# Performance work log

Measured on AMD Instinct MI355X. Metric: run time of the kernel, lower is better.

## Reference

```python
import jax, jax.numpy as jnp
import numpy as np
from jax import lax

VOCAB = 32000
D_MODEL = 1024
N_LAYERS = 4
D_STATE = 8
D_CONV = 4
EXPAND = 2
D_INNER = EXPAND * D_MODEL          # 2048
DT_RANK = (D_MODEL + 15) // 16      # 64
B, L = 2, 1024


def setup_inputs() -> dict:
    key = jax.random.key(0)
    ks = jax.random.split(key, 20)
    s = 0.02
    inp = {
        "input_ids": jax.random.randint(ks[0], (B, L), 0, VOCAB, dtype=jnp.int32),
        "embed": jax.random.normal(ks[1], (VOCAB, D_MODEL), jnp.float32) * s,
        "in_proj_w": jax.random.normal(ks[2], (N_LAYERS, 2 * D_INNER, D_MODEL), jnp.float32) * s,
        "conv_w": jax.random.normal(ks[3], (N_LAYERS, D_INNER, 1, D_CONV), jnp.float32) * s,
        "conv_b": jnp.zeros((N_LAYERS, D_INNER), jnp.float32),
        "x_proj_w": jax.random.normal(ks[4], (N_LAYERS, DT_RANK + 2 * D_STATE, D_INNER), jnp.float32) * s,
        "dt_proj_w": jax.random.normal(ks[5], (N_LAYERS, D_INNER, DT_RANK), jnp.float32) * s,
        "dt_proj_b": jax.random.normal(ks[6], (N_LAYERS, D_INNER), jnp.float32) * 0.1,
        "A_log": jnp.broadcast_to(jnp.log(jnp.arange(1, D_STATE + 1, dtype=jnp.float32)),
                                  (N_LAYERS, D_INNER, D_STATE)) + 0.0,
        "D": jnp.ones((N_LAYERS, D_INNER), jnp.float32),
        "out_proj_w": jax.random.normal(ks[7], (N_LAYERS, D_MODEL, D_INNER), jnp.float32) * s,
        "ln_g": jnp.ones((N_LAYERS, D_MODEL), jnp.float32),
        "ln_b": jnp.zeros((N_LAYERS, D_MODEL), jnp.float32),
        "fn_g": jnp.ones((D_MODEL,), jnp.float32),
        "fn_b": jnp.zeros((D_MODEL,), jnp.float32),
        "fc_w": jax.random.normal(ks[8], (VOCAB, D_MODEL), jnp.float32) * s,
        "fc_b": jnp.zeros((VOCAB,), jnp.float32),
    }
    return inp


def layer_norm(x, g, b, eps=1e-5):
    mu = jnp.mean(x, -1, keepdims=True)
    var = jnp.var(x, -1, keepdims=True)
    return (x - mu) * lax.rsqrt(var + eps) * g + b


def silu(x):
    return x * jax.nn.sigmoid(x)


def selective_scan(deltaA, deltaBu, C):
    # deltaA, deltaBu: (b,l,d,n); C: (b,l,n) -> y: (b,l,d)
    def step(h, inp):
        dA, dBu, c = inp
        h = dA * h + dBu                       # (b,d,n)
        y = jnp.einsum('bdn,bn->bd', h, c)
        return h, y
    h0 = jnp.zeros(deltaA.shape[:1] + deltaA.shape[2:], deltaA.dtype)
    _, ys = lax.scan(step, h0, (deltaA.transpose(1, 0, 2, 3),
                                deltaBu.transpose(1, 0, 2, 3),
                                C.transpose(1, 0, 2)))
    return ys.transpose(1, 0, 2)


def mamba_block(x, in_proj_w, conv_w, conv_b, x_proj_w, dt_proj_w, dt_proj_b, A_log, D, out_proj_w):
    # x: (b,l,d_model)
    xz = jnp.einsum('bld,ed->ble', x, in_proj_w)          # (b,l,2*di)
    xc, z = jnp.split(xz, 2, axis=-1)
    # causal depthwise conv1d, kernel D_CONV
    xc_ncl = xc.transpose(0, 2, 1)                         # (b,di,l)
    xc_ncl = lax.conv_general_dilated(
        xc_ncl, conv_w, window_strides=(1,), padding=[(D_CONV - 1, 0)],
        feature_group_count=D_INNER, dimension_numbers=('NCH', 'OIH', 'NCH'))
    xc = silu(xc_ncl.transpose(0, 2, 1) + conv_b)          # (b,l,di)
    x_dbl = jnp.einsum('bld,ed->ble', xc, x_proj_w)        # (b,l,dt_rank+2n)
    dt, Bm, Cm = jnp.split(x_dbl, [DT_RANK, DT_RANK + D_STATE], axis=-1)
    dt = jax.nn.softplus(jnp.einsum('blr,dr->bld', dt, dt_proj_w) + dt_proj_b)  # (b,l,di)
    A = -jnp.exp(A_log)                                    # (di,n)
    deltaA = jnp.exp(dt[..., None] * A)                    # (b,l,di,n)
    deltaBu = dt[..., None] * Bm[:, :, None, :] * xc[..., None]
    y = selective_scan(deltaA, deltaBu, Cm)                # (b,l,di)
    y = y + xc * D
    y = y * silu(z)
    return jnp.einsum('ble,de->bld', y, out_proj_w)


def reference(input_ids, embed, in_proj_w, conv_w, conv_b, x_proj_w, dt_proj_w,
              dt_proj_b, A_log, D, out_proj_w, ln_g, ln_b, fn_g, fn_b, fc_w, fc_b):
    x = embed[input_ids]                                   # (b,l,d)
    for i in range(N_LAYERS):
        out = mamba_block(x, in_proj_w[i], conv_w[i], conv_b[i], x_proj_w[i],
                          dt_proj_w[i], dt_proj_b[i], A_log[i], D[i], out_proj_w[i])
        x = layer_norm(out + x, ln_g[i], ln_b[i])
    x = layer_norm(x, fn_g, fn_b)
    logits = jnp.einsum('bld,vd->blv', x, fc_w) + fc_b
    return logits
```

## Files before the change

### kernel.cpp

```cpp
#include <hip/hip_runtime.h>
#include <cstddef>
#include <cstdint>

#define D_MODEL 1024
#define D_INNER 2048
#define DT_RANK 64
#define D_STATE 8
#define NLAYERS 4
#define BATCH 2
#define SEQ 1024
#define M_ROWS (BATCH*SEQ)
#define VOCAB 32000
#define XPAD 128
#define NC 32
#define LC 32
#define XSK 8

typedef __attribute__((ext_vector_type(8))) short short8;
typedef __attribute__((ext_vector_type(4))) float f32x4;

#define GPTR(p) (const __attribute__((address_space(1))) void*)(p)
#define LPTR(p) (__attribute__((address_space(3))) void*)(p)

__device__ __forceinline__ float sigmoidf_(float x) { return 1.f / (1.f + __expf(-x)); }

__device__ __forceinline__ unsigned short f2bf(float f) {
    unsigned u = __float_as_uint(f);
    u += 0x7fffu + ((u >> 16) & 1u);
    return (unsigned short)(u >> 16);
}
__device__ __forceinline__ float bf2f(unsigned short u) {
    return __uint_as_float((unsigned)u << 16);
}

__global__ __launch_bounds__(256) void cast_kernel(const float* __restrict__ in,
                                                   unsigned short* __restrict__ out, int n4)
{
    int i = blockIdx.x * 256 + threadIdx.x;
    if (i >= n4) return;
    float4 v = ((const float4*)in)[i];
    ushort4 o;
    o.x = f2bf(v.x); o.y = f2bf(v.y); o.z = f2bf(v.z); o.w = f2bf(v.w);
    ((ushort4*)out)[i] = o;
}

__global__ __launch_bounds__(256) void cast_pad_xproj(const float* __restrict__ in,
                                                      unsigned short* __restrict__ out)
{
    int i = blockIdx.x * 256 + threadIdx.x;
    if (i >= NLAYERS * XPAD * D_INNER / 4) return;
    int col4 = i & (D_INNER / 4 - 1);
    int row = (i >> 9) & (XPAD - 1);
    int layer = i >> 16;
    ushort4 o = {0, 0, 0, 0};
    if (row < 80) {
        float4 v = ((const float4*)(in + ((size_t)layer * 80 + row) * D_INNER))[col4];
        o.x = f2bf(v.x); o.y = f2bf(v.y); o.z = f2bf(v.z); o.w = f2bf(v.w);
    }
    ((ushort4*)out)[i] = o;
}

__global__ __launch_bounds__(256) void gather_kernel(const int* __restrict__ ids,
                                                     const float* __restrict__ embed,
                                                     float* __restrict__ x,
                                                     unsigned short* __restrict__ xb)
{
    int m = blockIdx.x;
    int t = threadIdx.x;
    int id = ids[m];
    float4 v = ((const float4*)(embed + (size_t)id * D_MODEL))[t];
    ((float4*)(x + (size_t)m * D_MODEL))[t] = v;
    ushort4 o;
    o.x = f2bf(v.x); o.y = f2bf(v.y); o.z = f2bf(v.z); o.w = f2bf(v.w);
    ((ushort4*)(xb + (size_t)m * D_MODEL))[t] = o;
}

template<int EPI>
__global__ __launch_bounds__(256) void gemm_bf16_nt(const unsigned short* __restrict__ A, int lda,
                                                    const unsigned short* __restrict__ B, int ldb,
                                                    void* __restrict__ Cv, int ldc,
                                                    int K, const float* __restrict__ bias)
{
    __shared__ unsigned short As[2][128 * 32];
    __shared__ unsigned short Bs[2][128 * 32];
    const int tid = threadIdx.x;

    const int gm = gridDim.x;
    const int bid = blockIdx.y * gm + blockIdx.x;
    const int q = (gm * gridDim.y) >> 3;
    const int swz = (bid & 7) * q + (bid >> 3);
    const int bm = (swz % gm) * 128, bn = (swz / gm) * 128;

    const int wid = tid >> 6, lane = tid & 63;
    const int wm = (wid >> 1) * 64, wn = (wid & 1) * 64;
    const int lrow = lane & 15, lkg = lane >> 4;

    const int srow = tid >> 2;
    const int ksrc = ((tid & 3) ^ ((srow >> 1) & 3)) * 8;
    const size_t kz = (size_t)blockIdx.z * K;
    const unsigned short* Ag = A + (size_t)(bm + srow) * lda + kz + ksrc;
    const unsigned short* Bg = B + (size_t)(bn + srow) * ldb + kz + ksrc;
    const size_t r64a = (size_t)64 * lda;
    const size_t r64b = (size_t)64 * ldb;

#define STAGE(buf, koff)                                                                              \
    do {                                                                                              \
        __builtin_amdgcn_global_load_lds(GPTR(Ag + (koff)),        LPTR(&As[buf][tid * 8]), 16, 0, 0);\
        __builtin_amdgcn_global_load_lds(GPTR(Ag + r64a + (koff)), LPTR(&As[buf][2048 + tid * 8]), 16, 0, 0);\
        __builtin_amdgcn_global_load_lds(GPTR(Bg + (koff)),        LPTR(&Bs[buf][tid * 8]), 16, 0, 0);\
        __builtin_amdgcn_global_load_lds(GPTR(Bg + r64b + (koff)), LPTR(&Bs[buf][2048 + tid * 8]), 16, 0, 0);\
    } while (0)

    f32x4 acc[4][4];
    #pragma unroll
    for (int i = 0; i < 4; ++i)
        #pragma unroll
        for (int j = 0; j < 4; ++j)
            acc[i][j] = f32x4{0.f, 0.f, 0.f, 0.f};

    STAGE(0, 0);

    int cur = 0;
    for (int k0 = 0; k0 < K; k0 += 32) {
        if (k0 + 32 < K) {
            STAGE(cur ^ 1, k0 + 32);
            asm volatile("s_waitcnt vmcnt(4)" ::: "memory");
        } else {
            asm volatile("s_waitcnt vmcnt(0)" ::: "memory");
        }
        __builtin_amdgcn_s_barrier();
        __builtin_amdgcn_sched_barrier(0);

        short8 af[4], bf[4];
        #pragma unroll
        for (int i = 0; i < 4; ++i) {
            int ra = wm + 16 * i + lrow;
            int pa = lkg ^ ((ra >> 1) & 3);
            af[i] = *(const short8*)(&As[cur][ra * 32 + pa * 8]);
            int rb = wn + 16 * i + lrow;
            int pb = lkg ^ ((rb >> 1) & 3);
            bf[i] = *(const short8*)(&Bs[cur][rb * 32 + pb * 8]);
        }
        __builtin_amdgcn_s_setprio(1);
        #pragma unroll
        for (int i = 0; i < 4; ++i)
            #pragma unroll
            for (int j = 0; j < 4; ++j)
                acc[i][j] = __builtin_amdgcn_mfma_f32_16x16x32_bf16(af[i], bf[j], acc[i][j], 0, 0, 0);
        __builtin_amdgcn_s_setprio(0);

        __builtin_amdgcn_s_barrier();
        cur ^= 1;
    }
#undef STAGE

    const int crow = bm + wm + lkg * 4;
    const int ccol = bn + wn + lrow;
    #pragma unroll
    for (int i = 0; i < 4; ++i) {
        #pragma unroll
        for (int j = 0; j < 4; ++j) {
            float bv = (EPI == 2 || EPI == 3) ? bias[ccol + 16 * j] : 0.f;
            #pragma unroll
            for (int r = 0; r < 4; ++r) {
                float v = acc[i][j][r] + bv;
                size_t off = (size_t)(crow + 16 * i + r) * ldc + ccol + 16 * j;
                if (EPI == 0) {
                    ((float*)Cv)[(size_t)blockIdx.z * M_ROWS * ldc + off] = v;
                } else if (EPI == 2) {
                    ((float*)Cv)[off] = v;
                } else {
                    if (EPI == 3) v = (v > 20.f) ? v : log1pf(__expf(v));
                    ((unsigned short*)Cv)[off] = f2bf(v);
                }
            }
        }
    }
}

__global__ __launch_bounds__(512) void gemm_bf16_nt256(const unsigned short* __restrict__ A, int lda,
                                                       const unsigned short* __restrict__ B, int ldb,
                                                       float* __restrict__ C, int ldc,
                                                       int K, const float* __restrict__ bias)
{
    __shared__ unsigned short As[2][256 * 32];
    __shared__ unsigned short Bs[2][256 * 32];
    const int tid = threadIdx.x;

    const int gm = gridDim.x;
    const int bid = blockIdx.y * gm + blockIdx.x;
    const int q = (gm * gridDim.y) >> 3;
    const int swz = (bid & 7) * q + (bid >> 3);
    const int bm = (swz % gm) * 256, bn = (swz / gm) * 256;

    const int wid = tid >> 6, lane = tid & 63;
    const int wm = (wid >> 2) * 128, wn = (wid & 3) * 64;
    const int lrow = lane & 15, lkg = lane >> 4;

    const int srow = tid >> 2;
    const int ksrc = ((tid & 3) ^ ((srow >> 1) & 3)) * 8;
    const unsigned short* Ag = A + (size_t)(bm + srow) * lda + ksrc;
    const unsigned short* Bg = B + (size_t)(bn + srow) * ldb + ksrc;
    const size_t r128a = (size_t)128 * lda;
    const size_t r128b = (size_t)128 * ldb;

#define STAGE2(buf, koff)                                                                               \
    do {                                                                                                \
        __builtin_amdgcn_global_load_lds(GPTR(Ag + (koff)),         LPTR(&As[buf][tid * 8]), 16, 0, 0); \
        __builtin_amdgcn_global_load_lds(GPTR(Ag + r128a + (koff)), LPTR(&As[buf][4096 + tid * 8]), 16, 0, 0);\
        __builtin_amdgcn_global_load_lds(GPTR(Bg + (koff)),         LPTR(&Bs[buf][tid * 8]), 16, 0, 0); \
        __builtin_amdgcn_global_load_lds(GPTR(Bg + r128b + (koff)), LPTR(&Bs[buf][4096 + tid * 8]), 16, 0, 0);\
    } while (0)

    f32x4 acc[8][4];
    #pragma unroll
    for (int i = 0; i < 8; ++i)
        #pragma unroll
        for (int j = 0; j < 4; ++j)
            acc[i][j] = f32x4{0.f, 0.f, 0.f, 0.f};

    STAGE2(0, 0);

    int cur = 0;
    for (int k0 = 0; k0 < K; k0 += 32) {
        if (k0 + 32 < K) {
            STAGE2(cur ^ 1, k0 + 32);
            asm volatile("s_waitcnt vmcnt(4)" ::: "memory");
        } else {
            asm volatile("s_waitcnt vmcnt(0)" ::: "memory");
        }
        __builtin_amdgcn_s_barrier();
        __builtin_amdgcn_sched_barrier(0);

        short8 af[8], bf[4];
        #pragma unroll
        for (int j = 0; j < 4; ++j) {
            int rb = wn + 16 * j + lrow;
            int pb = lkg ^ ((rb >> 1) & 3);
            bf[j] = *(const short8*)(&Bs[cur][rb * 32 + pb * 8]);
        }
        #pragma unroll
        for (int i = 0; i < 8; ++i) {
            int ra = wm + 16 * i + lrow;
            int pa = lkg ^ ((ra >> 1) & 3);
            af[i] = *(const short8*)(&As[cur][ra * 32 + pa * 8]);
        }
        __builtin_amdgcn_s_setprio(1);
        #pragma unroll
        for (int i = 0; i < 8; ++i)
            #pragma unroll
            for (int j = 0; j < 4; ++j)
                acc[i][j] = __builtin_amdgcn_mfma_f32_16x16x32_bf16(af[i], bf[j], acc[i][j], 0, 0, 0);
        __builtin_amdgcn_s_setprio(0);

        __builtin_amdgcn_s_barrier();
        cur ^= 1;
    }
#undef STAGE2

    const int crow = bm + wm + lkg * 4;
    const int ccol = bn + wn + lrow;
    #pragma unroll
    for (int i = 0; i < 8; ++i) {
        #pragma unroll
        for (int j = 0; j < 4; ++j) {
            float bv = bias[ccol + 16 * j];
            float* Cp = C + (size_t)(crow + 16 * i) * ldc + ccol + 16 * j;
            #pragma unroll
            for (int r = 0; r < 4; ++r)
                Cp[(size_t)r * ldc] = acc[i][j][r] + bv;
        }
    }
}

__global__ __launch_bounds__(256) void reduce_xdbl(const float* __restrict__ part,
                                                   float* __restrict__ xdbl,
                                                   unsigned short* __restrict__ xdbl_b)
{
    int i = blockIdx.x * 256 + threadIdx.x;
    float4 s = ((const float4*)part)[i];
    #pragma unroll
    for (int z = 1; z < XSK; ++z) {
        float4 v = ((const float4*)part)[(size_t)z * (M_ROWS * XPAD / 4) + i];
        s.x += v.x; s.y += v.y; s.z += v.z; s.w += v.w;
    }
    ((float4*)xdbl)[i] = s;
    ushort4 o;
    o.x = f2bf(s.x); o.y = f2bf(s.y); o.z = f2bf(s.z); o.w = f2bf(s.w);
    ((ushort4*)xdbl_b)[i] = o;
}

__global__ __launch_bounds__(256) void conv_silu_kernel(const unsigned short* __restrict__ xzb,
                                                        const float* __restrict__ cw,
                                                        const float* __restrict__ cb,
                                                        unsigned short* __restrict__ xcb)
{
    int idx = blockIdx.x * 256 + threadIdx.x;
    int d = idx & (D_INNER - 1);
    int m = idx >> 11;
    int l = m & (SEQ - 1);
    int b = m >> 10;
    float w0 = cw[d * 4 + 0], w1 = cw[d * 4 + 1], w2 = cw[d * 4 + 2], w3 = cw[d * 4 + 3];
    float s = cb[d];
    const unsigned short* base = xzb + ((size_t)b * SEQ) * (2 * D_INNER) + d;
    if (l - 3 >= 0) s += bf2f(base[(size_t)(l - 3) * (2 * D_INNER)]) * w0;
    if (l - 2 >= 0) s += bf2f(base[(size_t)(l - 2) * (2 * D_INNER)]) * w1;
    if (l - 1 >= 0) s += bf2f(base[(size_t)(l - 1) * (2 * D_INNER)]) * w2;
    s += bf2f(base[(size_t)l * (2 * D_INNER)]) * w3;
    float v = s * sigmoidf_(s);
    xcb[(size_t)m * D_INNER + d] = f2bf(v);
}

__global__ __launch_bounds__(256) void scan_partial(const unsigned short* __restrict__ dtb,
                                                    const float* __restrict__ xdbl,
                                                    const unsigned short* __restrict__ xcb,
                                                    const float* __restrict__ A_log,
                                                    float* __restrict__ H,
                                                    float* __restrict__ P)
{
    const int tid = threadIdx.x;
    const int b = blockIdx.x & 1;
    const int c = (blockIdx.x >> 1) & (NC - 1);
    const int d = ((blockIdx.x >> 6) << 8) + tid;

    __shared__ float Bsm[LC][8];
    {
        int r = tid >> 3, n = tid & 7;
        Bsm[r][n] = xdbl[(size_t)(b * SEQ + c * LC + r) * XPAD + DT_RANK + n];
    }
    __syncthreads();

    float An[8];
    #pragma unroll
    for (int n = 0; n < 8; ++n) An[n] = -__expf(A_log[d * 8 + n]);
    float h[8] = {0.f,0.f,0.f,0.f,0.f,0.f,0.f,0.f};
    float p[8] = {1.f,1.f,1.f,1.f,1.f,1.f,1.f,1.f};

    const unsigned short* dtp = dtb + (size_t)(b * SEQ + c * LC) * D_INNER + d;
    const unsigned short* xcp = xcb + (size_t)(b * SEQ + c * LC) * D_INNER + d;
    for (int l = 0; l < LC; ++l) {
        float dtv = bf2f(dtp[(size_t)l * D_INNER]);
        float ux  = dtv * bf2f(xcp[(size_t)l * D_INNER]);
        #pragma unroll
        for (int n = 0; n < 8; ++n) {
            float dA = __expf(dtv * An[n]);
            h[n] = dA * h[n] + Bsm[l][n] * ux;
            p[n] *= dA;
        }
    }
    size_t base = (size_t)((b * NC + c) * 8) * D_INNER + d;
    #pragma unroll
    for (int n = 0; n < 8; ++n) {
        H[base + (size_t)n * D_INNER] = h[n];
        P[base + (size_t)n * D_INNER] = p[n];
    }
}

__global__ __launch_bounds__(256) void scan_combine(const float* __restrict__ H,
                                                    float* __restrict__ P )
{
    int idx = blockIdx.x * 256 + threadIdx.x;
    int d = idx & (D_INNER - 1);
    int n = (idx >> 11) & 7;
    int b = idx >> 14;
    float hp = 0.f;
    for (int c = 0; c < NC; ++c) {
        size_t base = (size_t)((b * NC + c) * 8 + n) * D_INNER + d;
        float Pv = P[base], Hv = H[base];
        P[base] = hp;
        hp = Pv * hp + Hv;
    }
}

__global__ __launch_bounds__(256) void scan_final(const unsigned short* __restrict__ dtb,
                                                  const float* __restrict__ xdbl,
                                                  const unsigned short* __restrict__ xcb,
                                                  const unsigned short* __restrict__ xzb,
                                                  const float* __restrict__ A_log,
                                                  const float* __restrict__ Dp,
                                                  const float* __restrict__ h0,
                                                  unsigned short* __restrict__ yb)
{
    const int tid = threadIdx.x;
    const int b = blockIdx.x & 1;
    const int c = (blockIdx.x >> 1) & (NC - 1);
    const int d = ((blockIdx.x >> 6) << 8) + tid;

    __shared__ float Bsm[LC][8];
    __shared__ float Csm[LC][8];
    {
        int r = tid >> 3, n = tid & 7;
        size_t xrow = (size_t)(b * SEQ + c * LC + r) * XPAD;
        Bsm[r][n] = xdbl[xrow + DT_RANK + n];
        Csm[r][n] = xdbl[xrow + DT_RANK + 8 + n];
    }
    __syncthreads();

    float An[8], h[8];
    size_t base = (size_t)((b * NC + c) * 8) * D_INNER + d;
    #pragma unroll
    for (int n = 0; n < 8; ++n) {
        An[n] = -__expf(A_log[d * 8 + n]);
        h[n] = h0[base + (size_t)n * D_INNER];
    }
    const float Dv = Dp[d];

    const unsigned short* dtp = dtb + (size_t)(b * SEQ + c * LC) * D_INNER + d;
    const unsigned short* xcp = xcb + (size_t)(b * SEQ + c * LC) * D_INNER + d;
    const unsigned short* zp  = xzb + (size_t)(b * SEQ + c * LC) * (2 * D_INNER) + D_INNER + d;
    unsigned short* ybp = yb + (size_t)(b * SEQ + c * LC) * D_INNER + d;

    for (int l = 0; l < LC; ++l) {
        float dtv = bf2f(dtp[(size_t)l * D_INNER]);
        float xcv = bf2f(xcp[(size_t)l * D_INNER]);
        float zv  = bf2f(zp[(size_t)l * (2 * D_INNER)]);
        float ux = dtv * xcv;
        float acc = 0.f;
        #pragma unroll
        for (int n = 0; n < 8; ++n) {
            float dA = __expf(dtv * An[n]);
            h[n] = dA * h[n] + Bsm[l][n] * ux;
            acc += h[n] * Csm[l][n];
        }
        float yv = (acc + xcv * Dv) * (zv * sigmoidf_(zv));
        ybp[(size_t)l * D_INNER] = f2bf(yv);
    }
}

template<bool ADD>
__global__ __launch_bounds__(256) void ln_kernel(const float* __restrict__ extra,
                                                 const float* __restrict__ xin,
                                                 float* __restrict__ xout,
                                                 unsigned short* __restrict__ xbout,
                                                 const float* __restrict__ g,
                                                 const float* __restrict__ bb)
{
    int m = blockIdx.x;
    int t = threadIdx.x;
    float4 v = ((const float4*)(xin + (size_t)m * D_MODEL))[t];
    if (ADD) {
        float4 e = ((const float4*)(extra + (size_t)m * D_MODEL))[t];
        v.x += e.x; v.y += e.y; v.z += e.z; v.w += e.w;
    }
    float s  = v.x + v.y + v.z + v.w;
    float s2 = v.x * v.x + v.y * v.y + v.z * v.z + v.w * v.w;
    for (int off = 32; off; off >>= 1) {
        s  += __shfl_down(s, off);
        s2 += __shfl_down(s2, off);
    }
    __shared__ float red[8];
    int wid = t >> 6, lane = t & 63;
    if (lane == 0) { red[wid] = s; red[wid + 4] = s2; }
    __syncthreads();
    if (t == 0) {
        float a  = red[0] + red[1] + red[2] + red[3];
        float b2 = red[4] + red[5] + red[6] + red[7];
        float mu = a * (1.f / D_MODEL);
        red[0] = mu;
        red[4] = b2 * (1.f / D_MODEL) - mu * mu;
    }
    __syncthreads();
    float mu = red[0];
    float rs = rsqrtf(red[4] + 1e-5f);
    float4 gg = ((const float4*)g)[t];
    float4 bv = ((const float4*)bb)[t];
    float4 o;
    o.x = (v.x - mu) * rs * gg.x + bv.x;
    o.y = (v.y - mu) * rs * gg.y + bv.y;
    o.z = (v.z - mu) * rs * gg.z + bv.z;
    o.w = (v.w - mu) * rs * gg.w + bv.w;
    ((float4*)(xout + (size_t)m * D_MODEL))[t] = o;
    ushort4 ob;
    ob.x = f2bf(o.x); ob.y = f2bf(o.y); ob.z = f2bf(o.z); ob.w = f2bf(o.w);
    ((ushort4*)(xbout + (size_t)m * D_MODEL))[t] = ob;
}

extern "C" void kernel_launch(void* const* d_in, const int* in_sizes, int n_in,
                              void* d_out, int out_size, void* d_ws, size_t ws_size,
                              hipStream_t stream)
{
    const int*   ids      = (const int*)d_in[0];
    const float* embed    = (const float*)d_in[1];
    const float* in_proj  = (const float*)d_in[2];
    const float* conv_w   = (const float*)d_in[3];
    const float* conv_b   = (const float*)d_in[4];
    const float* x_proj   = (const float*)d_in[5];
    const float* dt_w     = (const float*)d_in[6];
    const float* dt_b     = (const float*)d_in[7];
    const float* A_log    = (const float*)d_in[8];
    const float* Dp       = (const float*)d_in[9];
    const float* out_proj = (const float*)d_in[10];
    const float* ln_g     = (const float*)d_in[11];
    const float* ln_b     = (const float*)d_in[12];
    const float* fn_g     = (const float*)d_in[13];
    const float* fn_b     = (const float*)d_in[14];
    const float* fc_w     = (const float*)d_in[15];
    const float* fc_b     = (const float*)d_in[16];
    float* logits = (float*)d_out;

    float* ws = (float*)d_ws;
    float* x     = ws;
    float* xdbl  = x + (size_t)M_ROWS * D_MODEL;
    float* tmp   = xdbl + (size_t)M_ROWS * XPAD;
    float* xpart = tmp + (size_t)M_ROWS * D_MODEL;

    float* Hbuf = tmp;
    float* Pbuf = tmp + (size_t)BATCH * NC * D_STATE * D_INNER;

    unsigned short* xb     = (unsigned short*)(xpart + (size_t)XSK * M_ROWS * XPAD);
    unsigned short* yb     = xb + (size_t)M_ROWS * D_MODEL;
    unsigned short* xzb    = yb + (size_t)M_ROWS * D_INNER;
    unsigned short* xcb    = xzb + (size_t)M_ROWS * 2 * D_INNER;
    unsigned short* dtb    = xcb + (size_t)M_ROWS * D_INNER;
    unsigned short* xdbl_b = dtb + (size_t)M_ROWS * D_INNER;
    unsigned short* wb_in  = xdbl_b + (size_t)M_ROWS * XPAD;
    unsigned short* wb_out = wb_in + (size_t)NLAYERS * 2 * D_INNER * D_MODEL;
    unsigned short* wb_fc  = wb_out + (size_t)NLAYERS * D_MODEL * D_INNER;
    unsigned short* wb_x   = wb_fc + (size_t)VOCAB * D_MODEL;
    unsigned short* wb_dt  = wb_x + (size_t)NLAYERS * XPAD * D_INNER;

    {
        int n4 = NLAYERS * 2 * D_INNER * D_MODEL / 4;
        cast_kernel<<<(n4 + 255) / 256, 256, 0, stream>>>(in_proj, wb_in, n4);
        n4 = NLAYERS * D_MODEL * D_INNER / 4;
        cast_kernel<<<(n4 + 255) / 256, 256, 0, stream>>>(out_proj, wb_out, n4);
        n4 = VOCAB * D_MODEL / 4;
        cast_kernel<<<(n4 + 255) / 256, 256, 0, stream>>>(fc_w, wb_fc, n4);
        n4 = NLAYERS * D_INNER * DT_RANK / 4;
        cast_kernel<<<(n4 + 255) / 256, 256, 0, stream>>>(dt_w, wb_dt, n4);
        n4 = NLAYERS * XPAD * D_INNER / 4;
        cast_pad_xproj<<<(n4 + 255) / 256, 256, 0, stream>>>(x_proj, wb_x);
    }

    gather_kernel<<<M_ROWS, 256, 0, stream>>>(ids, embed, x, xb);

    for (int i = 0; i < NLAYERS; ++i) {
        const unsigned short* W_in_b  = wb_in + (size_t)i * 2 * D_INNER * D_MODEL;
        const unsigned short* W_out_b = wb_out + (size_t)i * D_MODEL * D_INNER;
        const unsigned short* W_x_b   = wb_x + (size_t)i * XPAD * D_INNER;
        const unsigned short* W_dt_b  = wb_dt + (size_t)i * D_INNER * DT_RANK;
        const float* cw    = conv_w + (size_t)i * D_INNER * 4;
        const float* cb    = conv_b + (size_t)i * D_INNER;
        const float* b_dt  = dt_b + (size_t)i * D_INNER;
        const float* Al    = A_log + (size_t)i * D_INNER * D_STATE;
        const float* Dl    = Dp + (size_t)i * D_INNER;
        const float* g     = ln_g + (size_t)i * D_MODEL;
        const float* bb    = ln_b + (size_t)i * D_MODEL;

        gemm_bf16_nt<1><<<dim3(M_ROWS / 128, 2 * D_INNER / 128), 256, 0, stream>>>(
            xb, D_MODEL, W_in_b, D_MODEL, xzb, 2 * D_INNER, D_MODEL, nullptr);

        conv_silu_kernel<<<(M_ROWS * D_INNER) / 256, 256, 0, stream>>>(xzb, cw, cb, xcb);

        gemm_bf16_nt<0><<<dim3(M_ROWS / 128, 1, XSK), 256, 0, stream>>>(
            xcb, D_INNER, W_x_b, D_INNER, xpart, XPAD, D_INNER / XSK, nullptr);
        reduce_xdbl<<<(M_ROWS * XPAD / 4) / 256, 256, 0, stream>>>(xpart, xdbl, xdbl_b);

        gemm_bf16_nt<3><<<dim3(M_ROWS / 128, D_INNER / 128), 256, 0, stream>>>(
            xdbl_b, XPAD, W_dt_b, DT_RANK, dtb, D_INNER, DT_RANK, b_dt);

        scan_partial<<<BATCH * NC * (D_INNER / 256), 256, 0, stream>>>(
            dtb, xdbl, xcb, Al, Hbuf, Pbuf);
        scan_combine<<<(BATCH * D_STATE * D_INNER) / 256, 256, 0, stream>>>(Hbuf, Pbuf);
        scan_final<<<BATCH * NC * (D_INNER / 256), 256, 0, stream>>>(
            dtb, xdbl, xcb, xzb, Al, Dl, Pbuf, yb);

        gemm_bf16_nt<0><<<dim3(M_ROWS / 128, D_MODEL / 128), 256, 0, stream>>>(
            yb, D_INNER, W_out_b, D_INNER, tmp, D_MODEL, D_INNER, nullptr);

        ln_kernel<true><<<M_ROWS, 256, 0, stream>>>(tmp, x, x, xb, g, bb);
    }

    ln_kernel<false><<<M_ROWS, 256, 0, stream>>>(nullptr, x, tmp, xb, fn_g, fn_b);

    gemm_bf16_nt256<<<dim3(M_ROWS / 256, VOCAB / 256), 512, 0, stream>>>(
        xb, D_MODEL, wb_fc, D_MODEL, logits, VOCAB, D_MODEL, fc_b);
}
```

Before: 1.010 ms.

## Rewrite vocab GEMM as phased K=64 pipeline with interleaved LDS reads and MFMA

Replaces the 256x256 vocab-projection GEMM with a variant that stages K tiles of 64 instead of 32. Each tile is split into four MFMA quadrant phases separated by barriers, with LDS fragment reads for the next quadrant and the global-to-LDS loads for A and B staggered across phases. The aim is to overlap LDS traffic and global loads with matrix-core work and to halve the number of loop iterations and barriers per K. In exchange it doubles shared memory to 128KB, which limits occupancy, and adds more barriers per tile.

```diff
diff --git a/kernel.cpp b/kernel.cpp
--- a/kernel.cpp
+++ b/kernel.cpp
@@ -178,13 +178,34 @@
     }
 }
 
-__global__ __launch_bounds__(512) void gemm_bf16_nt256(const unsigned short* __restrict__ A, int lda,
-                                                       const unsigned short* __restrict__ B, int ldb,
-                                                       float* __restrict__ C, int ldc,
-                                                       int K, const float* __restrict__ bias)
-{
-    __shared__ unsigned short As[2][256 * 32];
-    __shared__ unsigned short Bs[2][256 * 32];
+__device__ __forceinline__ void rd_a8(const unsigned short* S, int base, int lrow, int lkg, short8 a[4][2]) {
+    #pragma unroll
+    for (int i = 0; i < 4; ++i)
+        #pragma unroll
+        for (int kk = 0; kk < 2; ++kk) {
+            int row = base + i * 16 + lrow;
+            int p = (kk * 4 + lkg) ^ (lrow & 7);
+            a[i][kk] = *(const short8*)(S + row * 64 + p * 8);
+        }
+}
+__device__ __forceinline__ void rd_b4(const unsigned short* S, int base, int lrow, int lkg, short8 b[2][2]) {
+    #pragma unroll
+    for (int j = 0; j < 2; ++j)
+        #pragma unroll
+        for (int kk = 0; kk < 2; ++kk) {
+            int row = base + j * 16 + lrow;
+            int p = (kk * 4 + lkg) ^ (lrow & 7);
+            b[j][kk] = *(const short8*)(S + row * 64 + p * 8);
+        }
+}
+
+__global__ __launch_bounds__(512) void gemm_bf16_8ph(const unsigned short* __restrict__ A, int lda,
+                                                     const unsigned short* __restrict__ B, int ldb,
+                                                     float* __restrict__ C, int ldc,
+                                                     int K, const float* __restrict__ bias)
+{
+    __shared__ unsigned short As[2][256 * 64];
+    __shared__ unsigned short Bs[2][256 * 64];
     const int tid = threadIdx.x;
 
     const int gm = gridDim.x;
@@ -194,23 +215,37 @@
     const int bm = (swz % gm) * 256, bn = (swz / gm) * 256;
 
     const int wid = tid >> 6, lane = tid & 63;
-    const int wm = (wid >> 2) * 128, wn = (wid & 3) * 64;
+    const int wr = wid >> 2, wc = wid & 3;
+    const int arow0 = wr * 128, brow0 = wc * 64;
     const int lrow = lane & 15, lkg = lane >> 4;
 
-    const int srow = tid >> 2;
-    const int ksrc = ((tid & 3) ^ ((srow >> 1) & 3)) * 8;
-    const unsigned short* Ag = A + (size_t)(bm + srow) * lda + ksrc;
-    const unsigned short* Bg = B + (size_t)(bn + srow) * ldb + ksrc;
-    const size_t r128a = (size_t)128 * lda;
-    const size_t r128b = (size_t)128 * ldb;
-
-#define STAGE2(buf, koff)                                                                               \
-    do {                                                                                                \
-        __builtin_amdgcn_global_load_lds(GPTR(Ag + (koff)),         LPTR(&As[buf][tid * 8]), 16, 0, 0); \
-        __builtin_amdgcn_global_load_lds(GPTR(Ag + r128a + (koff)), LPTR(&As[buf][4096 + tid * 8]), 16, 0, 0);\
-        __builtin_amdgcn_global_load_lds(GPTR(Bg + (koff)),         LPTR(&Bs[buf][tid * 8]), 16, 0, 0); \
-        __builtin_amdgcn_global_load_lds(GPTR(Bg + r128b + (koff)), LPTR(&Bs[buf][4096 + tid * 8]), 16, 0, 0);\
-    } while (0)
+    const int sg = tid >> 3, su = tid & 7;
+    const int ksrc = (su ^ (sg & 7)) * 8;
+    const unsigned short* Ag = A + (size_t)(bm + sg) * lda + ksrc;
+    const unsigned short* Bg = B + (size_t)(bn + sg) * ldb + ksrc;
+
+#define STG_A(buf, kt) do {                                                                                        \
+    __builtin_amdgcn_global_load_lds(GPTR(Ag + (size_t)(kt) * 64),                       LPTR(&As[buf][tid * 8]), 16, 0, 0); \
+    __builtin_amdgcn_global_load_lds(GPTR(Ag + (size_t)(kt) * 64 + (size_t)64 * lda),    LPTR(&As[buf][4096 + tid * 8]), 16, 0, 0); \
+    __builtin_amdgcn_global_load_lds(GPTR(Ag + (size_t)(kt) * 64 + (size_t)128 * lda),   LPTR(&As[buf][8192 + tid * 8]), 16, 0, 0); \
+    __builtin_amdgcn_global_load_lds(GPTR(Ag + (size_t)(kt) * 64 + (size_t)192 * lda),   LPTR(&As[buf][12288 + tid * 8]), 16, 0, 0); \
+} while (0)
+#define STG_B(buf, kt) do {                                                                                        \
+    __builtin_amdgcn_global_load_lds(GPTR(Bg + (size_t)(kt) * 64),                       LPTR(&Bs[buf][tid * 8]), 16, 0, 0); \
+    __builtin_amdgcn_global_load_lds(GPTR(Bg + (size_t)(kt) * 64 + (size_t)64 * ldb),    LPTR(&Bs[buf][4096 + tid * 8]), 16, 0, 0); \
+    __builtin_amdgcn_global_load_lds(GPTR(Bg + (size_t)(kt) * 64 + (size_t)128 * ldb),   LPTR(&Bs[buf][8192 + tid * 8]), 16, 0, 0); \
+    __builtin_amdgcn_global_load_lds(GPTR(Bg + (size_t)(kt) * 64 + (size_t)192 * ldb),   LPTR(&Bs[buf][12288 + tid * 8]), 16, 0, 0); \
+} while (0)
+#define MFMA_Q(IH, JH) do {                                                                                        \
+    __builtin_amdgcn_s_setprio(1);                                                                                 \
+    _Pragma("unroll") for (int i = 0; i < 4; ++i)                                                                  \
+    _Pragma("unroll") for (int j = 0; j < 2; ++j)                                                                  \
+    _Pragma("unroll") for (int kk = 0; kk < 2; ++kk)                                                               \
+        acc[(IH) * 4 + i][(JH) * 2 + j] =                                                                          \
+            __builtin_amdgcn_mfma_f32_16x16x32_bf16(a[i][kk], b[j][kk], acc[(IH) * 4 + i][(JH) * 2 + j], 0, 0, 0); \
+    __builtin_amdgcn_s_setprio(0);                                                                                 \
+} while (0)
+#define PBAR() __builtin_amdgcn_s_barrier()
 
     f32x4 acc[8][4];
     #pragma unroll
@@ -219,47 +254,47 @@
         for (int j = 0; j < 4; ++j)
             acc[i][j] = f32x4{0.f, 0.f, 0.f, 0.f};
 
-    STAGE2(0, 0);
-
-    int cur = 0;
-    for (int k0 = 0; k0 < K; k0 += 32) {
-        if (k0 + 32 < K) {
-            STAGE2(cur ^ 1, k0 + 32);
+    short8 a[4][2], b[2][2];
+    const int NT = K >> 6;
+
+    STG_A(0, 0); STG_B(0, 0); STG_A(1, 1);
+    asm volatile("s_waitcnt vmcnt(4)" ::: "memory");
+    PBAR();
+
+    int buf = 0;
+    for (int U = 0; U < NT; ++U, buf ^= 1) {
+        if (U + 1 < NT) STG_B(buf ^ 1, U + 1);
+        rd_a8(As[buf], arow0, lrow, lkg, a);
+        rd_b4(Bs[buf], brow0, lrow, lkg, b);
+        PBAR(); __builtin_amdgcn_sched_barrier(0);
+        MFMA_Q(0, 0);
+        PBAR();
+        rd_b4(Bs[buf], brow0 + 32, lrow, lkg, b);
+        PBAR(); __builtin_amdgcn_sched_barrier(0);
+        MFMA_Q(0, 1);
+        PBAR();
+        rd_a8(As[buf], arow0 + 64, lrow, lkg, a);
+        PBAR(); __builtin_amdgcn_sched_barrier(0);
+        MFMA_Q(1, 1);
+        PBAR();
+        rd_b4(Bs[buf], brow0, lrow, lkg, b);
+        if (U + 2 < NT) {
+            STG_A(buf, U + 2);
             asm volatile("s_waitcnt vmcnt(4)" ::: "memory");
         } else {
             asm volatile("s_waitcnt vmcnt(0)" ::: "memory");
         }
-        __builtin_amdgcn_s_barrier();
-        __builtin_amdgcn_sched_barrier(0);
-
-        short8 af[8], bf[4];
-        #pragma unroll
-        for (int j = 0; j < 4; ++j) {
-            int rb = wn + 16 * j + lrow;
-            int pb = lkg ^ ((rb >> 1) & 3);
-            bf[j] = *(const short8*)(&Bs[cur][rb * 32 + pb * 8]);
-        }
-        #pragma unroll
-        for (int i = 0; i < 8; ++i) {
-            int ra = wm + 16 * i + lrow;
-            int pa = lkg ^ ((ra >> 1) & 3);
-            af[i] = *(const short8*)(&As[cur][ra * 32 + pa * 8]);
-        }
-        __builtin_amdgcn_s_setprio(1);
-        #pragma unroll
-        for (int i = 0; i < 8; ++i)
-            #pragma unroll
-            for (int j = 0; j < 4; ++j)
-                acc[i][j] = __builtin_amdgcn_mfma_f32_16x16x32_bf16(af[i], bf[j], acc[i][j], 0, 0, 0);
-        __builtin_amdgcn_s_setprio(0);
-
-        __builtin_amdgcn_s_barrier();
-        cur ^= 1;
-    }
-#undef STAGE2
-
-    const int crow = bm + wm + lkg * 4;
-    const int ccol = bn + wn + lrow;
+        PBAR(); __builtin_amdgcn_sched_barrier(0);
+        MFMA_Q(1, 0);
+        PBAR();
+    }
+#undef STG_A
+#undef STG_B
+#undef MFMA_Q
+#undef PBAR
+
+    const int crow = bm + arow0 + lkg * 4;
+    const int ccol = bn + brow0 + lrow;
     #pragma unroll
     for (int i = 0; i < 8; ++i) {
         #pragma unroll
@@ -573,6 +608,6 @@
 
     ln_kernel<false><<<M_ROWS, 256, 0, stream>>>(nullptr, x, tmp, xb, fn_g, fn_b);
 
-    gemm_bf16_nt256<<<dim3(M_ROWS / 256, VOCAB / 256), 512, 0, stream>>>(
+    gemm_bf16_8ph<<<dim3(M_ROWS / 256, VOCAB / 256), 512, 0, stream>>>(
         xb, D_MODEL, wb_fc, D_MODEL, logits, VOCAB, D_MODEL, fc_b);
 }
```

Result: no change. 1.002 ms (-0.7%).
